# Optimization experiments

Measured on AMD Instinct MI355X. Metric: run time of the kernel, lower is better.

## Reference

```python
import jax, jax.numpy as jnp
import numpy as np

B, N, DIM = 4, 4096, 512
H, DH = 8, 64
INNER = H * DH
M = 256            # num_landmarks (N % M == 0, so no padding branch)
PINV_ITERS = 6
KERNEL = 33
EPS = 1e-8


def moore_penrose_iter_pinv(x, iters=PINV_ITERS):
    # x: [b, h, m, m]
    abs_x = jnp.abs(x)
    col = abs_x.sum(axis=-1)
    row = abs_x.sum(axis=-2)
    z = jnp.swapaxes(x, -1, -2) / (jnp.max(col) * jnp.max(row) + 1e-8)
    I = jnp.eye(x.shape[-1], dtype=x.dtype)
    for _ in range(iters):
        xz = x @ z
        z = 0.25 * z @ (13 * I - xz @ (15 * I - xz @ (7 * I - xz)))
    return z


def setup_inputs() -> dict:
    key = jax.random.key(0)
    kx, kqkv, kout, kres = jax.random.split(key, 4)
    x = jax.random.normal(kx, (B, N, DIM), dtype=jnp.float32)
    w_qkv = jax.random.normal(kqkv, (DIM, 3 * INNER), dtype=jnp.float32) * (DIM ** -0.5)
    w_out = jax.random.normal(kout, (INNER, DIM), dtype=jnp.float32) * (INNER ** -0.5)
    # depthwise Conv2d(heads, heads, (33,1), groups=heads): weight [H, 1, 33, 1]
    w_res = jax.random.normal(kres, (H, 1, KERNEL, 1), dtype=jnp.float32) * (KERNEL ** -0.5)
    return {"x": x, "w_qkv": w_qkv, "w_out": w_out, "w_res": w_res}


def reference(x, w_qkv, w_out, w_res):
    b, n, _ = x.shape
    l = n // M  # tokens per landmark group
    scale = DH ** -0.5

    qkv = x @ w_qkv                                   # [b, n, 3*inner]
    q, k, v = jnp.split(qkv, 3, axis=-1)
    def to_heads(t):
        return t.reshape(b, n, H, DH).transpose(0, 2, 1, 3)  # [b, h, n, d]
    q, k, v = to_heads(q), to_heads(k), to_heads(v)
    q = q * scale

    # landmarks: mean over consecutive groups of l tokens
    q_land = q.reshape(b, H, M, l, DH).sum(axis=3) / l      # [b, h, m, d]
    k_land = k.reshape(b, H, M, l, DH).sum(axis=3) / l

    sim1 = jnp.einsum('bhid,bhjd->bhij', q, k_land)         # [b, h, n, m]
    sim2 = jnp.einsum('bhid,bhjd->bhij', q_land, k_land)    # [b, h, m, m]
    sim3 = jnp.einsum('bhid,bhjd->bhij', q_land, k)         # [b, h, m, n]

    attn1 = jax.nn.softmax(sim1, axis=-1)
    attn2 = jax.nn.softmax(sim2, axis=-1)
    attn3 = jax.nn.softmax(sim3, axis=-1)

    attn2_inv = moore_penrose_iter_pinv(attn2)
    out = attn1 @ (attn2_inv @ (attn3 @ v))                 # [b, h, n, d]

    # residual depthwise conv over sequence dim, per head channel
    res = jax.lax.conv_general_dilated(
        v, w_res, window_strides=(1, 1),
        padding=((KERNEL // 2, KERNEL // 2), (0, 0)),
        dimension_numbers=('NCHW', 'OIHW', 'NCHW'),
        feature_group_count=H)
    out = out + res

    out = out.transpose(0, 2, 1, 3).reshape(b, n, INNER)    # [b, n, inner]
    out = out @ w_out                                       # [b, n, dim]
    return out[:, -n:]
```

## Files before the change

kernel.cpp:

```cpp
#include <hip/hip_runtime.h>


typedef __attribute__((ext_vector_type(8))) short bf16x8;
typedef __attribute__((ext_vector_type(4))) float f32x4;

constexpr size_t O_XP  = 0;
constexpr size_t O_QP  = 8388608;
constexpr size_t O_KP  = 16777216;
constexpr size_t O_VT  = 25165824;
constexpr size_t O_QL  = 33554432;
constexpr size_t O_KL  = 34078720;
constexpr size_t O_QLP = 34603008;
constexpr size_t O_KLP = 35127296;
constexpr size_t O_A2  = 35651584;
constexpr size_t O_T1  = 37748736;
constexpr size_t O_RS3 = 38273024;
constexpr size_t O_SCAL= 38281216;
constexpr size_t O_T2  = 38281232;
constexpr size_t O_WQT = 38805520;
constexpr size_t O_WOT = 39591952;
constexpr size_t O_END = 39854096;

__device__ __forceinline__ void split2(float x, unsigned short& h,
                                       unsigned short& l) {
    unsigned u  = __float_as_uint(x);
    unsigned hb = (u + 0x7FFFu + ((u >> 16) & 1u)) & 0xFFFF0000u;
    h = (unsigned short)(hb >> 16);
    float d = x - __uint_as_float(hb);
    l = (unsigned short)(__float_as_uint(d) >> 16);
}

__device__ __forceinline__ float b2f(unsigned short s) {
    return __uint_as_float((unsigned)s << 16);
}

__device__ __forceinline__ f32x4 mfma3(bf16x8 ah, bf16x8 al, bf16x8 bh,
                                       bf16x8 bl, f32x4 c) {
    c = __builtin_amdgcn_mfma_f32_16x16x32_bf16(ah, bh, c, 0, 0, 0);
    c = __builtin_amdgcn_mfma_f32_16x16x32_bf16(ah, bl, c, 0, 0, 0);
    c = __builtin_amdgcn_mfma_f32_16x16x32_bf16(al, bh, c, 0, 0, 0);
    return c;
}

__device__ __forceinline__ void stage_split4(float4 av, unsigned short* H,
                                             unsigned short* L, int off) {
    unsigned short h0, h1, h2, h3, l0, l1, l2, l3;
    split2(av.x, h0, l0); split2(av.y, h1, l1);
    split2(av.z, h2, l2); split2(av.w, h3, l3);
    uint2 ph, pl;
    ph.x = (unsigned)h0 | ((unsigned)h1 << 16);
    ph.y = (unsigned)h2 | ((unsigned)h3 << 16);
    pl.x = (unsigned)l0 | ((unsigned)l1 << 16);
    pl.y = (unsigned)l2 | ((unsigned)l3 << 16);
    *(uint2*)&H[off] = ph;
    *(uint2*)&L[off] = pl;
}

__global__ void xsplit(const float* __restrict__ X,
                       unsigned short* __restrict__ Xh,
                       unsigned short* __restrict__ Xl) {
    int idx = blockIdx.x * 256 + threadIdx.x;
    float4 v = *(const float4*)(X + (size_t)idx * 4);
    stage_split4(v, Xh, Xl, idx * 4);
}

__global__ void zinit_n(const float* __restrict__ a2,
                        const float* __restrict__ scal,
                        unsigned short* __restrict__ Zh,
                        unsigned short* __restrict__ Zl) {
    int idx = blockIdx.x * 256 + threadIdx.x;
    float denom = scal[0] * scal[1] + 1e-8f;
    int bh = idx >> 16, r = (idx >> 8) & 255, c = idx & 255;
    float v = a2[idx] / denom;
    unsigned short h, l;
    split2(v, h, l);
    size_t o = ((size_t)bh << 16) + ((size_t)c << 8) + r;
    Zh[o] = h;
    Zl[o] = l;
}

template <int EPI, bool ASCAL, bool WN, bool WTT>
__global__ __launch_bounds__(256) void mfma_gemm_p(
    const unsigned short* __restrict__ ANh, const unsigned short* __restrict__ ANl,
    const unsigned short* __restrict__ BTh, const unsigned short* __restrict__ BTl,
    unsigned short* __restrict__ CNh, unsigned short* __restrict__ CNl,
    unsigned short* __restrict__ CTh, unsigned short* __restrict__ CTl,
    float alpha, float beta, const float* __restrict__ scal) {
    __shared__ unsigned short Ah[64 * 40], Al[64 * 40];
    __shared__ unsigned short Bh[64 * 40], Bl[64 * 40];
    const int t = threadIdx.x;
    const int wave = t >> 6, lane = t & 63, lm = lane & 15, lq = lane >> 4;
    const int z = blockIdx.z;
    const int m0 = blockIdx.y * 64, n0 = blockIdx.x * 64;
    const size_t zo = (size_t)z * 65536;

    f32x4 acc[4];
#pragma unroll
    for (int j = 0; j < 4; ++j) acc[j] = (f32x4){0.f, 0.f, 0.f, 0.f};

    const int row = t >> 2, ko = (t & 3) * 8;
    for (int kt = 0; kt < 256; kt += 32) {
        *(uint4*)&Ah[row * 40 + ko] =
            *(const uint4*)(ANh + zo + (size_t)(m0 + row) * 256 + kt + ko);
        *(uint4*)&Al[row * 40 + ko] =
            *(const uint4*)(ANl + zo + (size_t)(m0 + row) * 256 + kt + ko);
        *(uint4*)&Bh[row * 40 + ko] =
            *(const uint4*)(BTh + zo + (size_t)(n0 + row) * 256 + kt + ko);
        *(uint4*)&Bl[row * 40 + ko] =
            *(const uint4*)(BTl + zo + (size_t)(n0 + row) * 256 + kt + ko);
        __syncthreads();
        bf16x8 ah = *(const bf16x8*)&Ah[(wave * 16 + lm) * 40 + lq * 8];
        bf16x8 al = *(const bf16x8*)&Al[(wave * 16 + lm) * 40 + lq * 8];
#pragma unroll
        for (int j = 0; j < 4; ++j) {
            bf16x8 bh = *(const bf16x8*)&Bh[(j * 16 + lm) * 40 + lq * 8];
            bf16x8 bl = *(const bf16x8*)&Bl[(j * 16 + lm) * 40 + lq * 8];
            acc[j] = mfma3(ah, al, bh, bl, acc[j]);
        }
        __syncthreads();
    }

    float a = alpha;
    if (ASCAL) a = 1.0f / (scal[0] * scal[1] + 1e-8f);
    const int r0 = m0 + wave * 16 + lq * 4;
#pragma unroll
    for (int j = 0; j < 4; ++j) {
        int c = n0 + j * 16 + lm;
        float vals[4];
#pragma unroll
        for (int e = 0; e < 4; ++e) {
            vals[e] = a * acc[j][e];
            if (EPI == 1) {
                size_t ao = zo + (size_t)(r0 + e) * 256 + c;
                vals[e] += beta * (b2f(ANh[ao]) + b2f(ANl[ao]));
            }
        }
        unsigned short hh[4], ll[4];
#pragma unroll
        for (int e = 0; e < 4; ++e) split2(vals[e], hh[e], ll[e]);
        if (WN) {
#pragma unroll
            for (int e = 0; e < 4; ++e) {
                size_t o = zo + (size_t)(r0 + e) * 256 + c;
                CNh[o] = hh[e];
                CNl[o] = ll[e];
            }
        }
        if (WTT) {
            uint2 ph, pl;
            ph.x = (unsigned)hh[0] | ((unsigned)hh[1] << 16);
            ph.y = (unsigned)hh[2] | ((unsigned)hh[3] << 16);
            pl.x = (unsigned)ll[0] | ((unsigned)ll[1] << 16);
            pl.y = (unsigned)ll[2] | ((unsigned)ll[3] << 16);
            *(uint2*)&CTh[zo + (size_t)c * 256 + r0] = ph;
            *(uint2*)&CTl[zo + (size_t)c * 256 + r0] = pl;
        }
    }
}

__device__ __forceinline__ void mt16(const float* As, const float* Bs,
                                     int ty4, int tx4, float (&acc)[4][4]) {
#pragma unroll
    for (int kk = 0; kk < 16; ++kk) {
        float4 a4 = *(const float4*)(As + kk * 68 + ty4);
        float4 b4 = *(const float4*)(Bs + kk * 68 + tx4);
        float aa[4] = {a4.x, a4.y, a4.z, a4.w};
        float bb[4] = {b4.x, b4.y, b4.z, b4.w};
#pragma unroll
        for (int u = 0; u < 4; ++u)
#pragma unroll
            for (int w = 0; w < 4; ++w)
                acc[u][w] += aa[u] * bb[w];
    }
}

__global__ __launch_bounds__(256) void t2_gemm(
    const unsigned short* __restrict__ ANh, const unsigned short* __restrict__ ANl,
    const float* __restrict__ t1, const float* __restrict__ rs3,
    float* __restrict__ t2, unsigned short* __restrict__ t2Th,
    unsigned short* __restrict__ t2Tl) {
    __shared__ float As[16 * 68];
    __shared__ float Bs[16 * 68];
    const int t  = threadIdx.x;
    const int z  = blockIdx.z;
    const int m0 = blockIdx.y * 64;
    const size_t zo = (size_t)z * 65536;
    const float* Bb = t1 + (size_t)z * 16384;
    float* Cb = t2 + (size_t)z * 16384;
    const int tx4 = (t & 15) * 4;
    const int ty4 = (t >> 4) * 4;
    const int ar  = t >> 2, ak = (t & 3) * 4;
    const int bkr = t >> 4, bc4 = (t & 15) * 4;
    float acc[4][4] = {};
    for (int kt = 0; kt < 256; kt += 16) {
        uint2 h2 = *(const uint2*)(ANh + zo + (size_t)(m0 + ar) * 256 + kt + ak);
        uint2 l2 = *(const uint2*)(ANl + zo + (size_t)(m0 + ar) * 256 + kt + ak);
        const unsigned short* hp = (const unsigned short*)&h2;
        const unsigned short* lp = (const unsigned short*)&l2;
        float4 av = make_float4(b2f(hp[0]) + b2f(lp[0]), b2f(hp[1]) + b2f(lp[1]),
                                b2f(hp[2]) + b2f(lp[2]), b2f(hp[3]) + b2f(lp[3]));
        float4 bv = *(const float4*)(Bb + (size_t)(kt + bkr) * 64 + bc4);
        float rr = 1.0f / rs3[z * 256 + kt + bkr];
        bv.x *= rr; bv.y *= rr; bv.z *= rr; bv.w *= rr;
        As[(ak + 0) * 68 + ar] = av.x;
        As[(ak + 1) * 68 + ar] = av.y;
        As[(ak + 2) * 68 + ar] = av.z;
        As[(ak + 3) * 68 + ar] = av.w;
        *(float4*)(Bs + bkr * 68 + bc4) = bv;
        __syncthreads();
        mt16(As, Bs, ty4, tx4, acc);
        __syncthreads();
    }
#pragma unroll
    for (int u = 0; u < 4; ++u) {
        int rowc = m0 + ty4 + u;
        *(float4*)(Cb + (size_t)rowc * 64 + tx4) =
            make_float4(acc[u][0], acc[u][1], acc[u][2], acc[u][3]);
    }
#pragma unroll
    for (int w = 0; w < 4; ++w) {
        unsigned short hh[4], ll[4];
#pragma unroll
        for (int u = 0; u < 4; ++u) split2(acc[u][w], hh[u], ll[u]);
        uint2 ph, pl;
        ph.x = (unsigned)hh[0] | ((unsigned)hh[1] << 16);
        ph.y = (unsigned)hh[2] | ((unsigned)hh[3] << 16);
        pl.x = (unsigned)ll[0] | ((unsigned)ll[1] << 16);
        pl.y = (unsigned)ll[2] | ((unsigned)ll[3] << 16);
        size_t off = (size_t)z * 16384 + (size_t)(tx4 + w) * 256 + m0 + ty4;
        *(uint2*)&t2Th[off] = ph;
        *(uint2*)&t2Tl[off] = pl;
    }
}

__global__ __launch_bounds__(256) void mfma_qkv(
    const unsigned short* __restrict__ Xh_, const unsigned short* __restrict__ Xl_,
    const unsigned short* __restrict__ WTh, const unsigned short* __restrict__ WTl,
    unsigned short* __restrict__ qh, unsigned short* __restrict__ ql,
    unsigned short* __restrict__ kh, unsigned short* __restrict__ kl,
    unsigned short* __restrict__ vTh, unsigned short* __restrict__ vTl) {
    __shared__ unsigned short Ah[128 * 40], Al[128 * 40];
    __shared__ unsigned short Bh[128 * 40], Bl[128 * 40];
    const int t = threadIdx.x;
    const int wave = t >> 6, lane = t & 63, lm = lane & 15, lq = lane >> 4;
    int orig = blockIdx.y * 12 + blockIdx.x;
    int wg = (orig & 7) * 192 + (orig >> 3);
    const int m0 = (wg / 12) * 128, n0 = (wg % 12) * 128;
    const int mb = (wave >> 1) * 64, nb = (wave & 1) * 64;
    f32x4 acc[4][4];
#pragma unroll
    for (int i = 0; i < 4; ++i)
#pragma unroll
        for (int j = 0; j < 4; ++j) acc[i][j] = (f32x4){0.f, 0.f, 0.f, 0.f};

    for (int kt = 0; kt < 512; kt += 32) {
#pragma unroll
        for (int r = 0; r < 2; ++r) {
            int id = t + r * 256, row = id >> 2, ko = (id & 3) * 8;
            *(uint4*)&Ah[row * 40 + ko] =
                *(const uint4*)(Xh_ + (size_t)(m0 + row) * 512 + kt + ko);
            *(uint4*)&Al[row * 40 + ko] =
                *(const uint4*)(Xl_ + (size_t)(m0 + row) * 512 + kt + ko);
        }
#pragma unroll
        for (int r = 0; r < 2; ++r) {
            int id = t + r * 256, row = id >> 2, ko = (id & 3) * 8;
            *(uint4*)&Bh[row * 40 + ko] =
                *(const uint4*)(WTh + (size_t)(n0 + row) * 512 + kt + ko);
            *(uint4*)&Bl[row * 40 + ko] =
                *(const uint4*)(WTl + (size_t)(n0 + row) * 512 + kt + ko);
        }
        __syncthreads();
        bf16x8 ah[4], al[4], bh[4], bl[4];
#pragma unroll
        for (int i = 0; i < 4; ++i) {
            ah[i] = *(const bf16x8*)&Ah[(mb + i * 16 + lm) * 40 + lq * 8];
            al[i] = *(const bf16x8*)&Al[(mb + i * 16 + lm) * 40 + lq * 8];
        }
#pragma unroll
        for (int j = 0; j < 4; ++j) {
            bh[j] = *(const bf16x8*)&Bh[(nb + j * 16 + lm) * 40 + lq * 8];
            bl[j] = *(const bf16x8*)&Bl[(nb + j * 16 + lm) * 40 + lq * 8];
        }
#pragma unroll
        for (int i = 0; i < 4; ++i)
#pragma unroll
            for (int j = 0; j < 4; ++j)
                acc[i][j] = mfma3(ah[i], al[i], bh[j], bl[j], acc[i][j]);
        __syncthreads();
    }
#pragma unroll
    for (int i = 0; i < 4; ++i)
#pragma unroll
        for (int j = 0; j < 4; ++j) {
            int r0 = m0 + mb + i * 16 + lq * 4;
            int c  = n0 + nb + j * 16 + lm;
            int which = c >> 9, h = (c >> 6) & 7, d = c & 63;
            int b = r0 >> 12, nbase = r0 & 4095;
            if (which == 2) {
                unsigned short hh[4], ll[4];
#pragma unroll
                for (int e = 0; e < 4; ++e) split2(acc[i][j][e], hh[e], ll[e]);
// ... 122 lines not shown
    __syncthreads();

    for (int c = c0; c < c0 + 8; ++c) {
        const int tok0 = c * 64;
#pragma unroll
        for (int r = 0; r < 2; ++r) {
            int id = t + r * 256, row = id >> 3, ko = (id & 7) * 8;
            *(uint4*)&Kh[row * 72 + ko] =
                *(const uint4*)(khb + (size_t)(tok0 + row) * 64 + ko);
            *(uint4*)&Kl[row * 72 + ko] =
                *(const uint4*)(klb + (size_t)(tok0 + row) * 64 + ko);
        }
        __syncthreads();
        bf16x8 a0  = *(const bf16x8*)&Qh[(wave * 16 + lm) * 72 + lq * 8];
        bf16x8 a0l = *(const bf16x8*)&Ql[(wave * 16 + lm) * 72 + lq * 8];
        bf16x8 a1  = *(const bf16x8*)&Qh[(wave * 16 + lm) * 72 + 32 + lq * 8];
        bf16x8 a1l = *(const bf16x8*)&Ql[(wave * 16 + lm) * 72 + 32 + lq * 8];
        f32x4 s[4];
#pragma unroll
        for (int j = 0; j < 4; ++j) s[j] = (f32x4){0.f, 0.f, 0.f, 0.f};
#pragma unroll
        for (int j = 0; j < 4; ++j) {
            bf16x8 b0  = *(const bf16x8*)&Kh[(j * 16 + lm) * 72 + lq * 8];
            bf16x8 b0l = *(const bf16x8*)&Kl[(j * 16 + lm) * 72 + lq * 8];
            bf16x8 b1  = *(const bf16x8*)&Kh[(j * 16 + lm) * 72 + 32 + lq * 8];
            bf16x8 b1l = *(const bf16x8*)&Kl[(j * 16 + lm) * 72 + 32 + lq * 8];
            s[j] = mfma3(a0, a0l, b0, b0l, s[j]);
            s[j] = mfma3(a1, a1l, b1, b1l, s[j]);
        }
        __syncthreads();
#pragma unroll
        for (int j = 0; j < 4; ++j)
#pragma unroll
            for (int e = 0; e < 4; ++e) {
                float ev = __expf(s[j][e]);
                rsum[e] += ev;
                unsigned short h, l;
                split2(ev, h, l);
                int off = (wave * 16 + lq * 4 + e) * 72 + j * 16 + lm;
                Eh[off] = h;
                El[off] = l;
            }
#pragma unroll
        for (int r = 0; r < 2; ++r) {
            int id = t + r * 256, dh = id >> 3, t8 = (id & 7) * 8;
            *(uint4*)&Kh[dh * 72 + t8] =
                *(const uint4*)(vhb + (size_t)dh * 4096 + tok0 + t8);
            *(uint4*)&Kl[dh * 72 + t8] =
                *(const uint4*)(vlb + (size_t)dh * 4096 + tok0 + t8);
        }
        __syncthreads();
        bf16x8 e0  = *(const bf16x8*)&Eh[(wave * 16 + lm) * 72 + lq * 8];
        bf16x8 e0l = *(const bf16x8*)&El[(wave * 16 + lm) * 72 + lq * 8];
        bf16x8 e1  = *(const bf16x8*)&Eh[(wave * 16 + lm) * 72 + 32 + lq * 8];
        bf16x8 e1l = *(const bf16x8*)&El[(wave * 16 + lm) * 72 + 32 + lq * 8];
#pragma unroll
        for (int j = 0; j < 4; ++j) {
            bf16x8 v0  = *(const bf16x8*)&Kh[(j * 16 + lm) * 72 + lq * 8];
            bf16x8 v0l = *(const bf16x8*)&Kl[(j * 16 + lm) * 72 + lq * 8];
            bf16x8 v1  = *(const bf16x8*)&Kh[(j * 16 + lm) * 72 + 32 + lq * 8];
            bf16x8 v1l = *(const bf16x8*)&Kl[(j * 16 + lm) * 72 + 32 + lq * 8];
            acc[j] = mfma3(e0, e0l, v0, v0l, acc[j]);
            acc[j] = mfma3(e1, e1l, v1, v1l, acc[j]);
        }
        __syncthreads();
    }
    float* t1b = t1 + (size_t)bz * 16384;
#pragma unroll
    for (int j = 0; j < 4; ++j)
#pragma unroll
        for (int e = 0; e < 4; ++e)
            atomicAdd(t1b + (size_t)(m0 + wave * 16 + lq * 4 + e) * 64 +
                          j * 16 + lm,
                      acc[j][e]);
#pragma unroll
    for (int e = 0; e < 4; ++e) {
        float vs = rsum[e];
        for (int mm = 1; mm < 16; mm <<= 1) vs += __shfl_xor(vs, mm);
        if (lm == 0)
            atomicAdd(rs3 + bz * 256 + m0 + wave * 16 + lq * 4 + e, vs);
    }
}

__global__ __launch_bounds__(256) void attn1t2_mfma(
    const unsigned short* __restrict__ qh_, const unsigned short* __restrict__ ql_,
    const unsigned short* __restrict__ klh, const unsigned short* __restrict__ kll,
    const unsigned short* __restrict__ t2Th,
    const unsigned short* __restrict__ t2Tl, float* __restrict__ oh) {
    __shared__ unsigned short Qh[4608], Ql[4608];
    __shared__ unsigned short Kh[4608], Kl[4608];
    __shared__ unsigned short Eh[4608], El[4608];
    const int t = threadIdx.x;
    const int wave = t >> 6, lane = t & 63, lm = lane & 15, lq = lane >> 4;
    const int bz = blockIdx.y, m0 = blockIdx.x * 64;
    const unsigned short* qhb = qh_ + (size_t)bz * 262144;
    const unsigned short* qlb = ql_ + (size_t)bz * 262144;
    const unsigned short* khb = klh + (size_t)bz * 16384;
    const unsigned short* klb = kll + (size_t)bz * 16384;
    const unsigned short* t2h = t2Th + (size_t)bz * 16384;
    const unsigned short* t2l = t2Tl + (size_t)bz * 16384;
#pragma unroll
    for (int r = 0; r < 2; ++r) {
        int id = t + r * 256, row = id >> 3, ko = (id & 7) * 8;
        *(uint4*)&Qh[row * 72 + ko] =
            *(const uint4*)(qhb + (size_t)(m0 + row) * 64 + ko);
        *(uint4*)&Ql[row * 72 + ko] =
            *(const uint4*)(qlb + (size_t)(m0 + row) * 64 + ko);
    }
    f32x4 acc[4];
#pragma unroll
    for (int j = 0; j < 4; ++j) acc[j] = (f32x4){0.f, 0.f, 0.f, 0.f};
    float rsum[4] = {0.f, 0.f, 0.f, 0.f};
    __syncthreads();

    for (int lc = 0; lc < 4; ++lc) {
        const int l0 = lc * 64;
#pragma unroll
        for (int r = 0; r < 2; ++r) {
            int id = t + r * 256, row = id >> 3, ko = (id & 7) * 8;
            *(uint4*)&Kh[row * 72 + ko] =
                *(const uint4*)(khb + (size_t)(l0 + row) * 64 + ko);
            *(uint4*)&Kl[row * 72 + ko] =
                *(const uint4*)(klb + (size_t)(l0 + row) * 64 + ko);
        }
        __syncthreads();
        bf16x8 a0  = *(const bf16x8*)&Qh[(wave * 16 + lm) * 72 + lq * 8];
        bf16x8 a0l = *(const bf16x8*)&Ql[(wave * 16 + lm) * 72 + lq * 8];
        bf16x8 a1  = *(const bf16x8*)&Qh[(wave * 16 + lm) * 72 + 32 + lq * 8];
        bf16x8 a1l = *(const bf16x8*)&Ql[(wave * 16 + lm) * 72 + 32 + lq * 8];
        f32x4 s[4];
#pragma unroll
        for (int j = 0; j < 4; ++j) s[j] = (f32x4){0.f, 0.f, 0.f, 0.f};
#pragma unroll
        for (int j = 0; j < 4; ++j) {
            bf16x8 b0  = *(const bf16x8*)&Kh[(j * 16 + lm) * 72 + lq * 8];
            bf16x8 b0l = *(const bf16x8*)&Kl[(j * 16 + lm) * 72 + lq * 8];
            bf16x8 b1  = *(const bf16x8*)&Kh[(j * 16 + lm) * 72 + 32 + lq * 8];
            bf16x8 b1l = *(const bf16x8*)&Kl[(j * 16 + lm) * 72 + 32 + lq * 8];
            s[j] = mfma3(a0, a0l, b0, b0l, s[j]);
            s[j] = mfma3(a1, a1l, b1, b1l, s[j]);
        }
        __syncthreads();
#pragma unroll
        for (int j = 0; j < 4; ++j)
#pragma unroll
            for (int e = 0; e < 4; ++e) {
                float ev = __expf(s[j][e]);
                rsum[e] += ev;
                unsigned short h, l;
                split2(ev, h, l);
                int off = (wave * 16 + lq * 4 + e) * 72 + j * 16 + lm;
                Eh[off] = h;
                El[off] = l;
            }
#pragma unroll
        for (int r = 0; r < 2; ++r) {
            int id = t + r * 256, dh = id >> 3, t8 = (id & 7) * 8;
            *(uint4*)&Kh[dh * 72 + t8] =
                *(const uint4*)(t2h + (size_t)dh * 256 + l0 + t8);
            *(uint4*)&Kl[dh * 72 + t8] =
                *(const uint4*)(t2l + (size_t)dh * 256 + l0 + t8);
        }
        __syncthreads();
        bf16x8 e0  = *(const bf16x8*)&Eh[(wave * 16 + lm) * 72 + lq * 8];
        bf16x8 e0l = *(const bf16x8*)&El[(wave * 16 + lm) * 72 + lq * 8];
        bf16x8 e1  = *(const bf16x8*)&Eh[(wave * 16 + lm) * 72 + 32 + lq * 8];
        bf16x8 e1l = *(const bf16x8*)&El[(wave * 16 + lm) * 72 + 32 + lq * 8];
#pragma unroll
        for (int j = 0; j < 4; ++j) {
            bf16x8 v0  = *(const bf16x8*)&Kh[(j * 16 + lm) * 72 + lq * 8];
            bf16x8 v0l = *(const bf16x8*)&Kl[(j * 16 + lm) * 72 + lq * 8];
            bf16x8 v1  = *(const bf16x8*)&Kh[(j * 16 + lm) * 72 + 32 + lq * 8];
            bf16x8 v1l = *(const bf16x8*)&Kl[(j * 16 + lm) * 72 + 32 + lq * 8];
            acc[j] = mfma3(e0, e0l, v0, v0l, acc[j]);
            acc[j] = mfma3(e1, e1l, v1, v1l, acc[j]);
        }
        __syncthreads();
    }
    float rinv[4];
#pragma unroll
    for (int e = 0; e < 4; ++e) {
        float vs = rsum[e];
        for (int mm = 1; mm < 16; mm <<= 1) vs += __shfl_xor(vs, mm);
        rinv[e] = 1.0f / vs;
    }
    float* ohb = oh + (size_t)bz * 262144;
#pragma unroll
    for (int j = 0; j < 4; ++j)
#pragma unroll
        for (int e = 0; e < 4; ++e)
            ohb[(size_t)(m0 + wave * 16 + lq * 4 + e) * 64 + j * 16 + lm] =
                acc[j][e] * rinv[e];
}

__global__ void wtrans(const float* __restrict__ W, int N,
                       unsigned short* __restrict__ Th,
                       unsigned short* __restrict__ Tl) {
    int idx = blockIdx.x * 256 + threadIdx.x;
    int n = idx >> 9, kk = idx & 511;
    float x = W[(size_t)kk * N + n];
    unsigned short h, l;
    split2(x, h, l);
    Th[idx] = h;
    Tl[idx] = l;
}

__global__ __launch_bounds__(256) void gemm_a2(
    const float* __restrict__ A, const float* __restrict__ B,
    float* __restrict__ C) {
    __shared__ float As[16 * 68];
    __shared__ float Bs[16 * 68];
    const int t  = threadIdx.x;
    const int z  = blockIdx.z;
    const int m0 = blockIdx.y * 64;
    const int n0 = blockIdx.x * 64;
    const float* Ab = A + (size_t)z * 16384;
    const float* Bb = B + (size_t)z * 16384;
    float*       Cb = C + (size_t)z * 65536;
    const int tx4 = (t & 15) * 4;
    const int ty4 = (t >> 4) * 4;
    const int ar  = t >> 2, ak = (t & 3) * 4;
    float acc[4][4] = {};
    for (int kt = 0; kt < 64; kt += 16) {
        float4 av = *(const float4*)(Ab + (size_t)(m0 + ar) * 64 + kt + ak);
        float4 bv = *(const float4*)(Bb + (size_t)(n0 + ar) * 64 + kt + ak);
        As[(ak + 0) * 68 + ar] = av.x;
        As[(ak + 1) * 68 + ar] = av.y;
        As[(ak + 2) * 68 + ar] = av.z;
        As[(ak + 3) * 68 + ar] = av.w;
        Bs[(ak + 0) * 68 + ar] = bv.x;
        Bs[(ak + 1) * 68 + ar] = bv.y;
        Bs[(ak + 2) * 68 + ar] = bv.z;
        Bs[(ak + 3) * 68 + ar] = bv.w;
        __syncthreads();
        mt16(As, Bs, ty4, tx4, acc);
        __syncthreads();
    }
#pragma unroll
    for (int u = 0; u < 4; ++u) {
        int row = m0 + ty4 + u;
        *(float4*)(Cb + (size_t)row * 256 + n0 + tx4) =
            make_float4(acc[u][0], acc[u][1], acc[u][2], acc[u][3]);
    }
}

__global__ void zero_f(float* __restrict__ p, int n) {
    int i = blockIdx.x * 256 + threadIdx.x;
    if (i < n) p[i] = 0.f;
}

__global__ void landmark_mean_p(const unsigned short* __restrict__ sh,
                                const unsigned short* __restrict__ sl,
                                float* __restrict__ dst,
                                unsigned short* __restrict__ dh,
                                unsigned short* __restrict__ dl) {
    int o = blockIdx.x * 256 + threadIdx.x;
    int d = o & 63, m = (o >> 6) & 255, bh = o >> 14;
    size_t base = (size_t)bh * 262144 + (size_t)m * 1024 + d;
    float acc = 0.f;
#pragma unroll
    for (int j = 0; j < 16; ++j)
        acc += b2f(sh[base + j * 64]) + b2f(sl[base + j * 64]);
    float v = acc * (1.0f / 16.0f);
    dst[o] = v;
    unsigned short h, l;
    split2(v, h, l);
    dh[o] = h;
    dl[o] = l;
}

__global__ void softmax_rows(float* __restrict__ a) {
    __shared__ float red[256];
    int row = blockIdx.x, t = threadIdx.x;
    float v = a[(size_t)row * 256 + t];
    red[t] = v;
    __syncthreads();
    for (int s = 128; s > 0; s >>= 1) {
        if (t < s) red[t] = fmaxf(red[t], red[t + s]);
        __syncthreads();
    }
    float mx = red[0];
    __syncthreads();
    float e = __expf(v - mx);
    red[t] = e;
    __syncthreads();
    for (int s = 128; s > 0; s >>= 1) {
        if (t < s) red[t] += red[t + s];
        __syncthreads();
    }
    a[(size_t)row * 256 + t] = e / red[0];
}

__global__ __launch_bounds__(256) void scalar_prep(const float* __restrict__ a,
                                                   float* __restrict__ scal) {
    __shared__ float red[256];
    int bh = blockIdx.x, t = threadIdx.x;
    const float* ab = a + (size_t)bh * 65536;
    float cs = 0.f;
    for (int i = 0; i < 256; ++i) cs += ab[i * 256 + t];
    red[t] = cs;
    __syncthreads();
    for (int s = 128; s > 0; s >>= 1) {
        if (t < s) red[t] = fmaxf(red[t], red[t + s]);
        __syncthreads();
    }
    float mcol = red[0];
    __syncthreads();
    float rs = 0.f;
    for (int j = 0; j < 256; ++j) rs += ab[t * 256 + j];
    red[t] = rs;
    __syncthreads();
    for (int s = 128; s > 0; s >>= 1) {
        if (t < s) red[t] = fmaxf(red[t], red[t + s]);
        __syncthreads();
    }
    if (t == 0) {
        atomicMax((unsigned int*)&scal[0], __float_as_uint(mcol));
        atomicMax((unsigned int*)&scal[1], __float_as_uint(red[0]));
    }
}

__global__ __launch_bounds__(256) void conv_tiled(
    const float* __restrict__ ohin, const unsigned short* __restrict__ vTh,
    const unsigned short* __restrict__ vTl, const float* __restrict__ wres,
    unsigned short* __restrict__ OHh, unsigned short* __restrict__ OHl) {
    __shared__ float Vs[160 * 65];
    __shared__ float Ws[33];
    const int t = threadIdx.x;
    const int bh = blockIdx.y;
    const int n0 = blockIdx.x * 128;
    const int h = bh & 7;
    if (t < 33) Ws[t] = wres[h * 33 + t];
    const unsigned short* vhb = vTh + (size_t)bh * 262144;
    const unsigned short* vlb = vTl + (size_t)bh * 262144;
#pragma unroll
    for (int r = 0; r < 5; ++r) {
        int id = t + r * 256;
        int d = id / 20, ch = id - d * 20;
        int n = n0 - 16 + ch * 8;
        uint4 h4 = make_uint4(0u, 0u, 0u, 0u);
        uint4 l4 = make_uint4(0u, 0u, 0u, 0u);
        if ((unsigned)n < 4096u) {
            h4 = *(const uint4*)(vhb + (size_t)d * 4096 + n);
            l4 = *(const uint4*)(vlb + (size_t)d * 4096 + n);
        }
        const unsigned short* hp = (const unsigned short*)&h4;
        const unsigned short* lp = (const unsigned short*)&l4;
        int row0 = ch * 8;
#pragma unroll
        for (int i = 0; i < 8; ++i)
            Vs[(row0 + i) * 65 + d] = b2f(hp[i]) + b2f(lp[i]);
    }
    __syncthreads();
    const int d = t & 63;
    const int g0 = (t >> 6) * 32;
    const float* ohb = ohin + (size_t)bh * 262144 + (size_t)n0 * 64;
    unsigned short* Hh = OHh + (size_t)bh * 262144 + (size_t)n0 * 64;
    unsigned short* Hl = OHl + (size_t)bh * 262144 + (size_t)n0 * 64;
    float w[33];
#pragma unroll
    for (int j = 0; j < 33; ++j) w[j] = Vs[(g0 + j) * 65 + d];
#pragma unroll
    for (int i = 0; i < 32; ++i) {
        float acc = ohb[(size_t)(g0 + i) * 64 + d];
#pragma unroll
        for (int tt = 0; tt < 33; ++tt) acc += w[tt] * Ws[tt];
        unsigned short hh, ll;
        split2(acc, hh, ll);
        Hh[(size_t)(g0 + i) * 64 + d] = hh;
        Hl[(size_t)(g0 + i) * 64 + d] = ll;
        if (i < 31) {
#pragma unroll
            for (int j = 0; j < 32; ++j) w[j] = w[j + 1];
            w[32] = Vs[(g0 + i + 33) * 65 + d];
        }
    }
}

extern "C" void kernel_launch(void* const* d_in, const int* in_sizes, int n_in,
                              void* d_out, int out_size, void* d_ws, size_t ws_size,
                              hipStream_t stream) {
    const float* x     = (const float*)d_in[0];
    const float* w_qkv = (const float*)d_in[1];
    const float* w_out = (const float*)d_in[2];
    const float* w_res = (const float*)d_in[3];
    float* out = (float*)d_out;
    float* ws  = (float*)d_ws;

    unsigned short* Xh  = (unsigned short*)(ws + O_XP);
    unsigned short* Xl  = Xh + 8388608;
    unsigned short* qh  = (unsigned short*)(ws + O_QP);
    unsigned short* ql  = qh + 8388608;
    unsigned short* kh  = (unsigned short*)(ws + O_KP);
    unsigned short* kl  = kh + 8388608;
    unsigned short* vTh = (unsigned short*)(ws + O_VT);
    unsigned short* vTl = vTh + 8388608;
    unsigned short* qlh = (unsigned short*)(ws + O_QLP);
    unsigned short* qll = qlh + 524288;
    unsigned short* klh = (unsigned short*)(ws + O_KLP);
    unsigned short* kll = klh + 524288;

    float* qland = ws + O_QL;
    float* kland = ws + O_KL;
    float* attn2 = ws + O_A2;
    float* t1    = ws + O_T1;
    float* rs3   = ws + O_RS3;
    float* scal  = ws + O_SCAL;
    float* t2    = ws + O_T2;

    unsigned short* PBu  = (unsigned short*)(ws + O_KP);
    unsigned short* A2Ph = PBu + 0;
    unsigned short* A2Pl = PBu + 2097152;
    unsigned short* XZNh = PBu + 4194304;
    unsigned short* XZNl = PBu + 6291456;
    unsigned short* XZTh = PBu + 8388608;
    unsigned short* XZTl = PBu + 10485760;
    unsigned short* Y1Th = PBu + 12582912;
    unsigned short* Y1Tl = PBu + 14680064;
    unsigned short* XRu  = (unsigned short*)(ws + O_XP);
    unsigned short* ZNah = XRu + 0;
    unsigned short* ZNal = XRu + 2097152;
    unsigned short* ZNbh = XRu + 4194304;
    unsigned short* ZNbl = XRu + 6291456;
    unsigned short* ZTh_ = XRu + 8388608;
    unsigned short* ZTl_ = XRu + 10485760;
    unsigned short* Y2Th = XRu + 12582912;
    unsigned short* Y2Tl = XRu + 14680064;
    unsigned short* t2Th = PBu;
    unsigned short* t2Tl = PBu + 524288;
    float* ohf = ws + O_XP;
    unsigned short* OHh = PBu;
    unsigned short* OHl = PBu + 8388608;

    unsigned short* WQTh = (unsigned short*)(ws + O_WQT);
    unsigned short* WQTl = WQTh + 786432;
    unsigned short* WOTh = (unsigned short*)(ws + O_WOT);
    unsigned short* WOTl = WOTh + 262144;

    zero_f<<<2081, 256, 0, stream>>>(t1, 532496);
    wtrans<<<3072, 256, 0, stream>>>(w_qkv, 1536, WQTh, WQTl);
    wtrans<<<1024, 256, 0, stream>>>(w_out, 512, WOTh, WOTl);
    xsplit<<<8192, 256, 0, stream>>>(x, Xh, Xl);

    mfma_qkv<<<dim3(12, 128), 256, 0, stream>>>(Xh, Xl, WQTh, WQTl,
                                                qh, ql, kh, kl, vTh, vTl);

    landmark_mean_p<<<2048, 256, 0, stream>>>(qh, ql, qland, qlh, qll);
    landmark_mean_p<<<2048, 256, 0, stream>>>(kh, kl, kland, klh, kll);

    gemm_a2<<<dim3(4, 4, 32), 256, 0, stream>>>(qland, kland, attn2);
    softmax_rows<<<8192, 256, 0, stream>>>(attn2);
    scalar_prep<<<32, 256, 0, stream>>>(attn2, scal);

    attn3v_mfma<<<dim3(8, 4, 32), 256, 0, stream>>>(qlh, qll, kh, kl,
                                                    vTh, vTl, t1, rs3);

    xsplit<<<2048, 256, 0, stream>>>(attn2, A2Ph, A2Pl);
    zinit_n<<<8192, 256, 0, stream>>>(attn2, scal, ZNah, ZNal);

    unsigned short* ZNh[2] = {ZNah, ZNbh};
    unsigned short* ZNl[2] = {ZNal, ZNbl};
    int cur = 0;
    const dim3 pg(4, 4, 32);
    for (int it = 0; it < 6; ++it) {
        if (it == 0) {
            mfma_gemm_p<0, true, true, true><<<pg, 256, 0, stream>>>(
                A2Ph, A2Pl, A2Ph, A2Pl, XZNh, XZNl, XZTh, XZTl,
                0.f, 0.f, scal);
        } else {
            mfma_gemm_p<0, false, true, true><<<pg, 256, 0, stream>>>(
                A2Ph, A2Pl, ZTh_, ZTl_, XZNh, XZNl, XZTh, XZTl,
                1.f, 0.f, nullptr);
        }
        mfma_gemm_p<1, false, false, true><<<pg, 256, 0, stream>>>(
            XZNh, XZNl, XZTh, XZTl, nullptr, nullptr, Y1Th, Y1Tl,
            -1.f, 7.f, nullptr);
        mfma_gemm_p<1, false, false, true><<<pg, 256, 0, stream>>>(
            XZNh, XZNl, Y1Th, Y1Tl, nullptr, nullptr, Y2Th, Y2Tl,
            -1.f, 15.f, nullptr);
        mfma_gemm_p<1, false, true, true><<<pg, 256, 0, stream>>>(
            ZNh[cur], ZNl[cur], Y2Th, Y2Tl, ZNh[1 - cur], ZNl[1 - cur],
            ZTh_, ZTl_, -0.25f, 3.25f, nullptr);
        cur = 1 - cur;
    }

    t2_gemm<<<dim3(1, 4, 32), 256, 0, stream>>>(ZNh[cur], ZNl[cur], t1, rs3,
                                                t2, t2Th, t2Tl);

    attn1t2_mfma<<<dim3(64, 32), 256, 0, stream>>>(qh, ql, klh, kll,
                                                   t2Th, t2Tl, ohf);

    conv_tiled<<<dim3(32, 32), 256, 0, stream>>>(ohf, vTh, vTl, w_res,
                                                 OHh, OHl);

    mfma_final<<<dim3(4, 128), 256, 0, stream>>>(OHh, OHl, WOTh, WOTl, out);

    (void)in_sizes; (void)n_in; (void)out_size; (void)ws_size;
}
```

Baseline: 841.3 us.

## Fuse softmax/pinv-init prep, merge weight transposes, fold conv into attn1 kernel

Merges the two weight-transpose launches and the two landmark-mean launches into single kernels. Softmax now writes the split bf16 hi/lo attn2 in both normal and transposed layouts and accumulates column sums atomically, which replaces scalar_prep, xsplit and zinit_n. Because softmax rows sum to one, the max row sum is dropped and the initial-Z scaling is applied in the first iteration's epilogue. The depthwise residual conv is fused into the attn1·t2 kernel so the fp32 intermediate output is neither written nor re-read. The cost is extra atomics and scattered transposed stores in softmax, plus more register and LDS pressure in the fused attention kernel.

```diff
diff --git a/kernel.cpp b/kernel.cpp
--- a/kernel.cpp
+++ b/kernel.cpp
@@ -16,7 +16,7 @@
 constexpr size_t O_T1  = 37748736;
 constexpr size_t O_RS3 = 38273024;
 constexpr size_t O_SCAL= 38281216;
-constexpr size_t O_T2  = 38281232;
+constexpr size_t O_CS  = 38281232;
 constexpr size_t O_WQT = 38805520;
 constexpr size_t O_WOT = 39591952;
 constexpr size_t O_END = 39854096;
@@ -64,22 +64,29 @@
     stage_split4(v, Xh, Xl, idx * 4);
 }
 
-__global__ void zinit_n(const float* __restrict__ a2,
-                        const float* __restrict__ scal,
-                        unsigned short* __restrict__ Zh,
-                        unsigned short* __restrict__ Zl) {
+__global__ void wtrans2(const float* __restrict__ Wq,
+                        const float* __restrict__ Wo,
+                        unsigned short* __restrict__ QTh,
+                        unsigned short* __restrict__ QTl,
+                        unsigned short* __restrict__ OTh,
+                        unsigned short* __restrict__ OTl) {
     int idx = blockIdx.x * 256 + threadIdx.x;
-    float denom = scal[0] * scal[1] + 1e-8f;
-    int bh = idx >> 16, r = (idx >> 8) & 255, c = idx & 255;
-    float v = a2[idx] / denom;
     unsigned short h, l;
-    split2(v, h, l);
-    size_t o = ((size_t)bh << 16) + ((size_t)c << 8) + r;
-    Zh[o] = h;
-    Zl[o] = l;
-}
-
-template <int EPI, bool ASCAL, bool WN, bool WTT>
+    if (idx < 786432) {
+        int n = idx >> 9, kk = idx & 511;
+        split2(Wq[(size_t)kk * 1536 + n], h, l);
+        QTh[idx] = h;
+        QTl[idx] = l;
+    } else {
+        int j = idx - 786432;
+        int n = j >> 9, kk = j & 511;
+        split2(Wo[(size_t)kk * 512 + n], h, l);
+        OTh[j] = h;
+        OTl[j] = l;
+    }
+}
+
+template <int EPI, int SC, bool WN, bool WTT>
 __global__ __launch_bounds__(256) void mfma_gemm_p(
     const unsigned short* __restrict__ ANh, const unsigned short* __restrict__ ANl,
     const unsigned short* __restrict__ BTh, const unsigned short* __restrict__ BTl,
@@ -120,8 +127,8 @@
         __syncthreads();
     }
 
-    float a = alpha;
-    if (ASCAL) a = 1.0f / (scal[0] * scal[1] + 1e-8f);
+    const float scv = (SC != 0) ? 1.0f / (scal[0] + 1e-8f) : 1.0f;
+    const float a = (SC == 1) ? scv : alpha;
     const int r0 = m0 + wave * 16 + lq * 4;
 #pragma unroll
     for (int j = 0; j < 4; ++j) {
@@ -129,11 +136,13 @@
         float vals[4];
 #pragma unroll
         for (int e = 0; e < 4; ++e) {
-            vals[e] = a * acc[j][e];
+            float v = a * acc[j][e];
             if (EPI == 1) {
                 size_t ao = zo + (size_t)(r0 + e) * 256 + c;
-                vals[e] += beta * (b2f(ANh[ao]) + b2f(ANl[ao]));
+                v += beta * (b2f(ANh[ao]) + b2f(ANl[ao]));
             }
+            if (SC == 2) v *= scv;
+            vals[e] = v;
         }
         unsigned short hh[4], ll[4];
 #pragma unroll
@@ -177,8 +186,7 @@
 __global__ __launch_bounds__(256) void t2_gemm(
     const unsigned short* __restrict__ ANh, const unsigned short* __restrict__ ANl,
     const float* __restrict__ t1, const float* __restrict__ rs3,
-    float* __restrict__ t2, unsigned short* __restrict__ t2Th,
-    unsigned short* __restrict__ t2Tl) {
+    unsigned short* __restrict__ t2Th, unsigned short* __restrict__ t2Tl) {
     __shared__ float As[16 * 68];
     __shared__ float Bs[16 * 68];
     const int t  = threadIdx.x;
@@ -186,7 +194,6 @@
     const int m0 = blockIdx.y * 64;
     const size_t zo = (size_t)z * 65536;
     const float* Bb = t1 + (size_t)z * 16384;
-    float* Cb = t2 + (size_t)z * 16384;
     const int tx4 = (t & 15) * 4;
     const int ty4 = (t >> 4) * 4;
     const int ar  = t >> 2, ak = (t & 3) * 4;
@@ -212,12 +219,6 @@
         __syncthreads();
     }
 #pragma unroll
-    for (int u = 0; u < 4; ++u) {
-        int rowc = m0 + ty4 + u;
-        *(float4*)(Cb + (size_t)rowc * 64 + tx4) =
-            make_float4(acc[u][0], acc[u][1], acc[u][2], acc[u][3]);
-    }
-#pragma unroll
     for (int w = 0; w < 4; ++w) {
         unsigned short hh[4], ll[4];
 #pragma unroll
@@ -506,17 +507,25 @@
     }
 }
 
-__global__ __launch_bounds__(256) void attn1t2_mfma(
+__global__ __launch_bounds__(256) void attn1t2_conv(
     const unsigned short* __restrict__ qh_, const unsigned short* __restrict__ ql_,
     const unsigned short* __restrict__ klh, const unsigned short* __restrict__ kll,
-    const unsigned short* __restrict__ t2Th,
-    const unsigned short* __restrict__ t2Tl, float* __restrict__ oh) {
-    __shared__ unsigned short Qh[4608], Ql[4608];
-    __shared__ unsigned short Kh[4608], Kl[4608];
-    __shared__ unsigned short Eh[4608], El[4608];
+    const unsigned short* __restrict__ t2Th, const unsigned short* __restrict__ t2Tl,
+    const unsigned short* __restrict__ vTh, const unsigned short* __restrict__ vTl,
+    const float* __restrict__ wres,
+    unsigned short* __restrict__ OHh, unsigned short* __restrict__ OHl) {
+    __shared__ __align__(16) unsigned short SH[27648];
+    unsigned short* Qh = SH;
+    unsigned short* Ql = SH + 4608;
+    unsigned short* Kh = SH + 9216;
+    unsigned short* Kl = SH + 13824;
+    unsigned short* Eh = SH + 18432;
+    unsigned short* El = SH + 23040;
+    __shared__ float Ws[33];
     const int t = threadIdx.x;
     const int wave = t >> 6, lane = t & 63, lm = lane & 15, lq = lane >> 4;
     const int bz = blockIdx.y, m0 = blockIdx.x * 64;
+    if (t < 33) Ws[t] = wres[(bz & 7) * 33 + t];
     const unsigned short* qhb = qh_ + (size_t)bz * 262144;
     const unsigned short* qlb = ql_ + (size_t)bz * 262144;
     const unsigned short* khb = klh + (size_t)bz * 16384;
@@ -608,25 +617,51 @@
         for (int mm = 1; mm < 16; mm <<= 1) vs += __shfl_xor(vs, mm);
         rinv[e] = 1.0f / vs;
     }
-    float* ohb = oh + (size_t)bz * 262144;
-#pragma unroll
-    for (int j = 0; j < 4; ++j)
-#pragma unroll
-        for (int e = 0; e < 4; ++e)
-            ohb[(size_t)(m0 + wave * 16 + lq * 4 + e) * 64 + j * 16 + lm] =
-                acc[j][e] * rinv[e];
-}
-
-__global__ void wtrans(const float* __restrict__ W, int N,
-                       unsigned short* __restrict__ Th,
-                       unsigned short* __restrict__ Tl) {
-    int idx = blockIdx.x * 256 + threadIdx.x;
-    int n = idx >> 9, kk = idx & 511;
-    float x = W[(size_t)kk * N + n];
-    unsigned short h, l;
-    split2(x, h, l);
-    Th[idx] = h;
-    Tl[idx] = l;
+
+    __syncthreads();
+    float* Vs = (float*)SH;
+    const unsigned short* vhb = vTh + (size_t)bz * 262144;
+    const unsigned short* vlb = vTl + (size_t)bz * 262144;
+#pragma unroll
+    for (int r = 0; r < 3; ++r) {
+        int id = t + r * 256;
+        int d = id / 12, ch = id - d * 12;
+        int n = m0 - 16 + ch * 8;
+        uint4 h4 = make_uint4(0u, 0u, 0u, 0u);
+        uint4 l4 = make_uint4(0u, 0u, 0u, 0u);
+        if ((unsigned)n < 4096u) {
+            h4 = *(const uint4*)(vhb + (size_t)d * 4096 + n);
+            l4 = *(const uint4*)(vlb + (size_t)d * 4096 + n);
+        }
+        const unsigned short* hp = (const unsigned short*)&h4;
+        const unsigned short* lp = (const unsigned short*)&l4;
+#pragma unroll
+        for (int i = 0; i < 8; ++i)
+            Vs[(ch * 8 + i) * 65 + d] = b2f(hp[i]) + b2f(lp[i]);
+    }
+    __syncthreads();
+    unsigned short* Hh = OHh + (size_t)bz * 262144;
+    unsigned short* Hl = OHl + (size_t)bz * 262144;
+    const int rbase = wave * 16 + lq * 4;
+#pragma unroll
+    for (int j = 0; j < 4; ++j) {
+        int cc = j * 16 + lm;
+        float w[36];
+#pragma unroll
+        for (int u = 0; u < 36; ++u) w[u] = Vs[(rbase + u) * 65 + cc];
+#pragma unroll
+        for (int e = 0; e < 4; ++e) {
+            float cv = 0.f;
+#pragma unroll
+            for (int tt = 0; tt < 33; ++tt) cv += w[e + tt] * Ws[tt];
+            float o = acc[j][e] * rinv[e] + cv;
+            unsigned short hh, ll;
+            split2(o, hh, ll);
+            size_t off = (size_t)(m0 + rbase + e) * 64 + cc;
+            Hh[off] = hh;
+            Hl[off] = ll;
+        }
+    }
 }
 
 __global__ __launch_bounds__(256) void gemm_a2(
@@ -673,27 +708,40 @@
     if (i < n) p[i] = 0.f;
 }
 
-__global__ void landmark_mean_p(const unsigned short* __restrict__ sh,
-                                const unsigned short* __restrict__ sl,
-                                float* __restrict__ dst,
-                                unsigned short* __restrict__ dh,
-                                unsigned short* __restrict__ dl) {
+__global__ void landmark_mean2(
+    const unsigned short* __restrict__ qh, const unsigned short* __restrict__ ql,
+    const unsigned short* __restrict__ kh, const unsigned short* __restrict__ kl,
+    float* __restrict__ qland, float* __restrict__ kland,
+    unsigned short* __restrict__ qlh, unsigned short* __restrict__ qll,
+    unsigned short* __restrict__ klh, unsigned short* __restrict__ kll) {
     int o = blockIdx.x * 256 + threadIdx.x;
-    int d = o & 63, m = (o >> 6) & 255, bh = o >> 14;
+    bool isq = o < 524288;
+    int oo = isq ? o : o - 524288;
+    const unsigned short* sh = isq ? qh : kh;
+    const unsigned short* sl = isq ? ql : kl;
+    float* dst = isq ? qland : kland;
+    unsigned short* dh = isq ? qlh : klh;
+    unsigned short* dl = isq ? qll : kll;
+    int d = oo & 63, m = (oo >> 6) & 255, bh = oo >> 14;
     size_t base = (size_t)bh * 262144 + (size_t)m * 1024 + d;
     float acc = 0.f;
 #pragma unroll
     for (int j = 0; j < 16; ++j)
         acc += b2f(sh[base + j * 64]) + b2f(sl[base + j * 64]);
     float v = acc * (1.0f / 16.0f);
-    dst[o] = v;
+    dst[oo] = v;
     unsigned short h, l;
     split2(v, h, l);
-    dh[o] = h;
-    dl[o] = l;
-}
-
-__global__ void softmax_rows(float* __restrict__ a) {
+    dh[oo] = h;
+    dl[oo] = l;
+}
+
+__global__ void softmax_fused(const float* __restrict__ a,
+                              unsigned short* __restrict__ A2Ph,
+                              unsigned short* __restrict__ A2Pl,
+                              unsigned short* __restrict__ A2Th,
+                              unsigned short* __restrict__ A2Tl,
+                              float* __restrict__ colsum) {
     __shared__ float red[256];
     int row = blockIdx.x, t = threadIdx.x;
     float v = a[(size_t)row * 256 + t];
@@ -712,93 +760,29 @@
         if (t < s) red[t] += red[t + s];
         __syncthreads();
     }
-    a[(size_t)row * 256 + t] = e / red[0];
-}
-
-__global__ __launch_bounds__(256) void scalar_prep(const float* __restrict__ a,
-                                                   float* __restrict__ scal) {
+    float val = e / red[0];
+    int z = row >> 8, r = row & 255;
+    atomicAdd(&colsum[z * 256 + t], val);
+    unsigned short h, l;
+    split2(val, h, l);
+    size_t zo = (size_t)z * 65536;
+    A2Ph[zo + (size_t)r * 256 + t] = h;
+    A2Pl[zo + (size_t)r * 256 + t] = l;
+    A2Th[zo + (size_t)t * 256 + r] = h;
+    A2Tl[zo + (size_t)t * 256 + r] = l;
+}
+
+__global__ void scal_max(const float* __restrict__ colsum,
+                         float* __restrict__ scal) {
     __shared__ float red[256];
-    int bh = blockIdx.x, t = threadIdx.x;
-    const float* ab = a + (size_t)bh * 65536;
-    float cs = 0.f;
-    for (int i = 0; i < 256; ++i) cs += ab[i * 256 + t];
-    red[t] = cs;
+    int t = threadIdx.x;
+    red[t] = colsum[blockIdx.x * 256 + t];
     __syncthreads();
     for (int s = 128; s > 0; s >>= 1) {
         if (t < s) red[t] = fmaxf(red[t], red[t + s]);
         __syncthreads();
     }
-    float mcol = red[0];
-    __syncthreads();
-    float rs = 0.f;
-    for (int j = 0; j < 256; ++j) rs += ab[t * 256 + j];
-    red[t] = rs;
-    __syncthreads();
-    for (int s = 128; s > 0; s >>= 1) {
-        if (t < s) red[t] = fmaxf(red[t], red[t + s]);
-        __syncthreads();
-    }
-    if (t == 0) {
-        atomicMax((unsigned int*)&scal[0], __float_as_uint(mcol));
-        atomicMax((unsigned int*)&scal[1], __float_as_uint(red[0]));
-    }
-}
-
-__global__ __launch_bounds__(256) void conv_tiled(
-    const float* __restrict__ ohin, const unsigned short* __restrict__ vTh,
-    const unsigned short* __restrict__ vTl, const float* __restrict__ wres,
-    unsigned short* __restrict__ OHh, unsigned short* __restrict__ OHl) {
-    __shared__ float Vs[160 * 65];
-    __shared__ float Ws[33];
-    const int t = threadIdx.x;
-    const int bh = blockIdx.y;
-    const int n0 = blockIdx.x * 128;
-    const int h = bh & 7;
-    if (t < 33) Ws[t] = wres[h * 33 + t];
-    const unsigned short* vhb = vTh + (size_t)bh * 262144;
-    const unsigned short* vlb = vTl + (size_t)bh * 262144;
-#pragma unroll
-    for (int r = 0; r < 5; ++r) {
-        int id = t + r * 256;
-        int d = id / 20, ch = id - d * 20;
-        int n = n0 - 16 + ch * 8;
-        uint4 h4 = make_uint4(0u, 0u, 0u, 0u);
-        uint4 l4 = make_uint4(0u, 0u, 0u, 0u);
-        if ((unsigned)n < 4096u) {
-            h4 = *(const uint4*)(vhb + (size_t)d * 4096 + n);
-            l4 = *(const uint4*)(vlb + (size_t)d * 4096 + n);
-        }
-        const unsigned short* hp = (const unsigned short*)&h4;
-        const unsigned short* lp = (const unsigned short*)&l4;
-        int row0 = ch * 8;
-#pragma unroll
-        for (int i = 0; i < 8; ++i)
-            Vs[(row0 + i) * 65 + d] = b2f(hp[i]) + b2f(lp[i]);
-    }
-    __syncthreads();
-    const int d = t & 63;
-    const int g0 = (t >> 6) * 32;
-    const float* ohb = ohin + (size_t)bh * 262144 + (size_t)n0 * 64;
-    unsigned short* Hh = OHh + (size_t)bh * 262144 + (size_t)n0 * 64;
-    unsigned short* Hl = OHl + (size_t)bh * 262144 + (size_t)n0 * 64;
-    float w[33];
-#pragma unroll
-    for (int j = 0; j < 33; ++j) w[j] = Vs[(g0 + j) * 65 + d];
-#pragma unroll
-    for (int i = 0; i < 32; ++i) {
-        float acc = ohb[(size_t)(g0 + i) * 64 + d];
-#pragma unroll
-        for (int tt = 0; tt < 33; ++tt) acc += w[tt] * Ws[tt];
-        unsigned short hh, ll;
-        split2(acc, hh, ll);
-        Hh[(size_t)(g0 + i) * 64 + d] = hh;
-        Hl[(size_t)(g0 + i) * 64 + d] = ll;
-        if (i < 31) {
-#pragma unroll
-            for (int j = 0; j < 32; ++j) w[j] = w[j + 1];
-            w[32] = Vs[(g0 + i + 33) * 65 + d];
-        }
-    }
+    if (t == 0) atomicMax((unsigned int*)&scal[0], __float_as_uint(red[0]));
 }
 
 extern "C" void kernel_launch(void* const* d_in, const int* in_sizes, int n_in,
@@ -830,7 +814,7 @@
     float* t1    = ws + O_T1;
     float* rs3   = ws + O_RS3;
     float* scal  = ws + O_SCAL;
-    float* t2    = ws + O_T2;
+    float* colsum= ws + O_CS;
 
     unsigned short* PBu  = (unsigned short*)(ws + O_KP);
     unsigned short* A2Ph = PBu + 0;
@@ -850,9 +834,10 @@
     unsigned short* ZTl_ = XRu + 10485760;
     unsigned short* Y2Th = XRu + 12582912;
     unsigned short* Y2Tl = XRu + 14680064;
-    unsigned short* t2Th = PBu;
-    unsigned short* t2Tl = PBu + 524288;
-    float* ohf = ws + O_XP;
+    unsigned short* A2Th = ZNah;
+    unsigned short* A2Tl = ZNal;
+    unsigned short* t2Th = (unsigned short*)(ws + O_QL);
+    unsigned short* t2Tl = t2Th + 524288;
     unsigned short* OHh = PBu;
     unsigned short* OHl = PBu + 8388608;
 
@@ -861,26 +846,23 @@
     unsigned short* WOTh = (unsigned short*)(ws + O_WOT);
     unsigned short* WOTl = WOTh + 262144;
 
-    zero_f<<<2081, 256, 0, stream>>>(t1, 532496);
-    wtrans<<<3072, 256, 0, stream>>>(w_qkv, 1536, WQTh, WQTl);
-    wtrans<<<1024, 256, 0, stream>>>(w_out, 512, WOTh, WOTl);
+    zero_f<<<2113, 256, 0, stream>>>(t1, 540688);
+    wtrans2<<<4096, 256, 0, stream>>>(w_qkv, w_out, WQTh, WQTl, WOTh, WOTl);
     xsplit<<<8192, 256, 0, stream>>>(x, Xh, Xl);
 
     mfma_qkv<<<dim3(12, 128), 256, 0, stream>>>(Xh, Xl, WQTh, WQTl,
                                                 qh, ql, kh, kl, vTh, vTl);
 
-    landmark_mean_p<<<2048, 256, 0, stream>>>(qh, ql, qland, qlh, qll);
-    landmark_mean_p<<<2048, 256, 0, stream>>>(kh, kl, kland, klh, kll);
-
-    gemm_a2<<<dim3(4, 4, 32), 256, 0, stream>>>(qland, kland, attn2);
-    softmax_rows<<<8192, 256, 0, stream>>>(attn2);
-    scalar_prep<<<32, 256, 0, stream>>>(attn2, scal);
+    landmark_mean2<<<4096, 256, 0, stream>>>(qh, ql, kh, kl, qland, kland,
+                                             qlh, qll, klh, kll);
 
     attn3v_mfma<<<dim3(8, 4, 32), 256, 0, stream>>>(qlh, qll, kh, kl,
                                                     vTh, vTl, t1, rs3);
 
-    xsplit<<<2048, 256, 0, stream>>>(attn2, A2Ph, A2Pl);
-    zinit_n<<<8192, 256, 0, stream>>>(attn2, scal, ZNah, ZNal);
+    gemm_a2<<<dim3(4, 4, 32), 256, 0, stream>>>(qland, kland, attn2);
+    softmax_fused<<<8192, 256, 0, stream>>>(attn2, A2Ph, A2Pl, A2Th, A2Tl,
+                                            colsum);
+    scal_max<<<32, 256, 0, stream>>>(colsum, scal);
 
     unsigned short* ZNh[2] = {ZNah, ZNbh};
     unsigned short* ZNl[2] = {ZNal, ZNbl};
@@ -888,34 +870,39 @@
     const dim3 pg(4, 4, 32);
     for (int it = 0; it < 6; ++it) {
         if (it == 0) {
-            mfma_gemm_p<0, true, true, true><<<pg, 256, 0, stream>>>(
+            mfma_gemm_p<0, 1, true, true><<<pg, 256, 0, stream>>>(
                 A2Ph, A2Pl, A2Ph, A2Pl, XZNh, XZNl, XZTh, XZTl,
                 0.f, 0.f, scal);
         } else {
-            mfma_gemm_p<0, false, true, true><<<pg, 256, 0, stream>>>(
+            mfma_gemm_p<0, 0, true, true><<<pg, 256, 0, stream>>>(
                 A2Ph, A2Pl, ZTh_, ZTl_, XZNh, XZNl, XZTh, XZTl,
-                1.f, 0.f, nullptr);
-        }
-        mfma_gemm_p<1, false, false, true><<<pg, 256, 0, stream>>>(
+                1.f, 0.f, scal);
+        }
+        mfma_gemm_p<1, 0, false, true><<<pg, 256, 0, stream>>>(
             XZNh, XZNl, XZTh, XZTl, nullptr, nullptr, Y1Th, Y1Tl,
-            -1.f, 7.f, nullptr);
-        mfma_gemm_p<1, false, false, true><<<pg, 256, 0, stream>>>(
+            -1.f, 7.f, scal);
+        mfma_gemm_p<1, 0, false, true><<<pg, 256, 0, stream>>>(
             XZNh, XZNl, Y1Th, Y1Tl, nullptr, nullptr, Y2Th, Y2Tl,
-            -1.f, 15.f, nullptr);
-        mfma_gemm_p<1, false, true, true><<<pg, 256, 0, stream>>>(
-            ZNh[cur], ZNl[cur], Y2Th, Y2Tl, ZNh[1 - cur], ZNl[1 - cur],
-            ZTh_, ZTl_, -0.25f, 3.25f, nullptr);
-        cur = 1 - cur;
-    }
-
-    t2_gemm<<<dim3(1, 4, 32), 256, 0, stream>>>(ZNh[cur], ZNl[cur], t1, rs3,
-                                                t2, t2Th, t2Tl);
-
-    attn1t2_mfma<<<dim3(64, 32), 256, 0, stream>>>(qh, ql, klh, kll,
-                                                   t2Th, t2Tl, ohf);
-
-    conv_tiled<<<dim3(32, 32), 256, 0, stream>>>(ohf, vTh, vTl, w_res,
-                                                 OHh, OHl);
+            -1.f, 15.f, scal);
+        if (it == 0) {
+            mfma_gemm_p<1, 2, true, true><<<pg, 256, 0, stream>>>(
+                A2Th, A2Tl, Y2Th, Y2Tl, ZNbh, ZNbl, ZTh_, ZTl_,
+                -0.25f, 3.25f, scal);
+            cur = 1;
+        } else {
+            mfma_gemm_p<1, 0, true, true><<<pg, 256, 0, stream>>>(
+                ZNh[cur], ZNl[cur], Y2Th, Y2Tl, ZNh[1 - cur], ZNl[1 - cur],
+                ZTh_, ZTl_, -0.25f, 3.25f, scal);
+            cur = 1 - cur;
+        }
+    }
+
+    t2_gemm<<<dim3(1, 4, 32), 256, 0, stream>>>(ZNh[0], ZNl[0], t1, rs3,
+                                                t2Th, t2Tl);
+
+    attn1t2_conv<<<dim3(64, 32), 256, 0, stream>>>(qh, ql, klh, kll,
+                                                   t2Th, t2Tl, vTh, vTl,
+                                                   w_res, OHh, OHl);
 
     mfma_final<<<dim3(4, 128), 256, 0, stream>>>(OHh, OHl, WOTh, WOTl, out);
 
```

New measurement: 834.7 us. About the same (-0.8%).
